# Kernel tuning notes

Hardware: AMD Instinct MI355X
Metric: run time of the kernel (lower is better)

## Reference

```python
import jax, jax.numpy as jnp
import numpy as np
from jax.ops import segment_sum

N_NODES = 100000
N_EDGES = 3200000
NUM_FEATURES = 256


def setup_inputs() -> dict:
    key = jax.random.key(0)
    ks = jax.random.split(key, 12)
    def lin(k, fan_in, fan_out):
        bound = 1.0 / np.sqrt(fan_in)
        kw, kb = jax.random.split(k)
        W = jax.random.uniform(kw, (fan_in, fan_out), jnp.float32, -bound, bound)
        b = jax.random.uniform(kb, (fan_out,), jnp.float32, -bound, bound)
        return W, b
    x = jax.random.normal(ks[0], (N_NODES, NUM_FEATURES), jnp.float32)
    edge_index = jax.random.randint(ks[1], (2, N_EDGES), 0, N_NODES, jnp.int64 if jax.config.jax_enable_x64 else jnp.int32)
    W1, b1 = lin(ks[2], NUM_FEATURES, 64)
    W2, b2 = lin(ks[3], 64, 32)
    W3, b3 = lin(ks[4], 32, 16)
    Ws02, bs02 = lin(ks[5], NUM_FEATURES, 32)
    Ws03, bs03 = lin(ks[6], NUM_FEATURES, 16)
    Ws13, bs13 = lin(ks[7], 64, 16)
    Wout, bout = lin(ks[8], 16, 1)
    return dict(x=x, edge_index=edge_index, W1=W1, b1=b1, W2=W2, b2=b2,
                W3=W3, b3=b3, Ws02=Ws02, bs02=bs02, Ws03=Ws03, bs03=bs03,
                Ws13=Ws13, bs13=bs13, Wout=Wout, bout=bout)


def _deg_inv_sqrt(edge_index, n_nodes):
    # gcn_norm with self-loops: degree counted at target nodes, +1 for self-loop
    dst = edge_index[1]
    deg = segment_sum(jnp.ones(edge_index.shape[1], jnp.float32), dst, num_segments=n_nodes) + 1.0
    return jnp.where(deg > 0, jax.lax.rsqrt(deg), 0.0)


def _gcn_conv(x, W, b, edge_index, dinv):
    # PyG GCNConv: h = x W; out[i] = sum_{j->i} dinv[j]*dinv[i]*h[j] + dinv[i]^2*h[i] + b
    src, dst = edge_index[0], edge_index[1]
    h = x @ W                                   # [N, out]
    norm = (dinv[src] * dinv[dst])[:, None]     # [E, 1]
    agg = segment_sum(h[src] * norm, dst, num_segments=x.shape[0])
    agg = agg + (dinv * dinv)[:, None] * h      # self-loop term
    return agg + b


def reference(x, edge_index, W1, b1, W2, b2, W3, b3,
              Ws02, bs02, Ws03, bs03, Ws13, bs13, Wout, bout):
    # Dropout in eval mode (identity).
    dinv = _deg_inv_sqrt(edge_index, x.shape[0])
    x1 = jax.nn.relu(_gcn_conv(x, W1, b1, edge_index, dinv))
    x2 = jax.nn.relu(_gcn_conv(x1, W2, b2, edge_index, dinv) + x @ Ws02 + bs02)
    x3 = jax.nn.relu(_gcn_conv(x2, W3, b3, edge_index, dinv)
                     + x @ Ws03 + bs03 + x1 @ Ws13 + bs13)
    return jax.nn.sigmoid(x3 @ Wout + bout)
```

## Files before the change

### kernel.cpp

```cpp
#include <hip/hip_runtime.h>
#include <hip/hip_bf16.h>
#include <math.h>


#define NBUCK_MAX 512
#define P1_CHUNK 8192
#define EPT 32
#define BCAP 9216

typedef __attribute__((ext_vector_type(8))) short bfrag;
typedef __attribute__((ext_vector_type(4))) float f4_t;

__device__ inline float uaf(unsigned u) { return __uint_as_float(u); }
__device__ inline ushort f2bf(float f) {
    __hip_bfloat16 b = __float2bfloat16(f);
    return *reinterpret_cast<ushort*>(&b);
}


__global__ __launch_bounds__(256) void bucket_hist_kernel(
    const int* __restrict__ dst, int E, int* __restrict__ bucket_count, int nbuckets)
{
    __shared__ int lhist[NBUCK_MAX];
    for (int i = threadIdx.x; i < nbuckets; i += 256) lhist[i] = 0;
    __syncthreads();
    const int stride = gridDim.x * 256;
    for (int e = blockIdx.x * 256 + threadIdx.x; e < E; e += stride)
        atomicAdd(&lhist[dst[e] >> 8], 1);
    __syncthreads();
    for (int i = threadIdx.x; i < nbuckets; i += 256) {
        int c = lhist[i];
        if (c) atomicAdd(&bucket_count[i], c);
    }
}

__global__ __launch_bounds__(512) void bucket_scan_kernel(
    const int* __restrict__ bucket_count, int* __restrict__ bucket_base,
    int* __restrict__ bucket_cursor, int nbuckets)
{
    __shared__ int tmp[512];
    const int tid = threadIdx.x;
    int v = (tid < nbuckets) ? bucket_count[tid] : 0;
    tmp[tid] = v;
    __syncthreads();
    for (int off = 1; off < 512; off <<= 1) {
        int t = (tid >= off) ? tmp[tid - off] : 0;
        __syncthreads();
        tmp[tid] += t;
        __syncthreads();
    }
    if (tid < nbuckets) {
        int base = tmp[tid] - v;
        bucket_base[tid]   = base;
        bucket_cursor[tid] = base;
    }
}

__global__ __launch_bounds__(256) void partition_kernel(
    const int* __restrict__ src, const int* __restrict__ dst, int E,
    int* __restrict__ bucket_cursor, unsigned int* __restrict__ keys, int nbuckets)
{
    __shared__ int hist[NBUCK_MAX];
    __shared__ int lofs[NBUCK_MAX];
    __shared__ int gbase[NBUCK_MAX];
    __shared__ int lcur[NBUCK_MAX];
    __shared__ int ssum[256];
    __shared__ unsigned int stage[P1_CHUNK];
    __shared__ int gidx[P1_CHUNK];

    const int tid = threadIdx.x;
    const int e0  = blockIdx.x * P1_CHUNK;
    const int nE  = min(P1_CHUNK, E - e0);

    for (int i = tid; i < NBUCK_MAX; i += 256) { hist[i] = 0; lcur[i] = 0; }
    __syncthreads();

    int myb[EPT];
    unsigned int mypk[EPT];
#pragma unroll
    for (int j = 0; j < EPT; ++j) {
        const int e = e0 + tid + j * 256;
        if (e < E) {
            const int d = dst[e];
            myb[j]  = d >> 8;
            mypk[j] = ((unsigned int)(d & 255) << 17) | (unsigned int)src[e];
            atomicAdd(&hist[myb[j]], 1);
        } else myb[j] = -1;
    }
    __syncthreads();

    int a0 = (2 * tid     < nbuckets) ? hist[2 * tid]     : 0;
    int a1 = (2 * tid + 1 < nbuckets) ? hist[2 * tid + 1] : 0;
    ssum[tid] = a0 + a1;
    __syncthreads();
    for (int off = 1; off < 256; off <<= 1) {
        int t = (tid >= off) ? ssum[tid - off] : 0;
        __syncthreads();
        ssum[tid] += t;
        __syncthreads();
    }
    const int ex = ssum[tid] - (a0 + a1);
    if (2 * tid     < nbuckets) lofs[2 * tid]     = ex;
    if (2 * tid + 1 < nbuckets) lofs[2 * tid + 1] = ex + a0;
    __syncthreads();

    for (int i = tid; i < nbuckets; i += 256)
        gbase[i] = atomicAdd(&bucket_cursor[i], hist[i]);
    __syncthreads();

#pragma unroll
    for (int j = 0; j < EPT; ++j) {
        if (myb[j] >= 0) {
            const int b = myb[j];
            const int l = lofs[b] + atomicAdd(&lcur[b], 1);
            stage[l] = mypk[j];
            gidx[l]  = gbase[b] - lofs[b] + l;
        }
    }
    __syncthreads();

    for (int i = tid; i < nE; i += 256)
        keys[gidx[i]] = stage[i];
}

__global__ __launch_bounds__(256) void csr_build_kernel(
    const unsigned int* __restrict__ keys, const int* __restrict__ bucket_base,
    const int* __restrict__ bucket_count,
    int* __restrict__ row_off, float* __restrict__ dinv, int* __restrict__ col,
    int N, int E)
{
    __shared__ unsigned int inb[BCAP];
    __shared__ int outv[BCAP];
    __shared__ int hist[256];
    __shared__ int lofs[256];
    __shared__ int ssum[256];

    const int tid  = threadIdx.x;
    const int b    = blockIdx.x;
    const int base = bucket_base[b];
    const int cnt  = min(bucket_count[b], BCAP);
    const int n0   = b << 8;
    const int nn   = min(256, N - n0);

    for (int i = tid; i < cnt; i += 256) inb[i] = keys[base + i];
    hist[tid] = 0;
    __syncthreads();

    for (int i = tid; i < cnt; i += 256)
        atomicAdd(&hist[inb[i] >> 17], 1);
    __syncthreads();

    ssum[tid] = hist[tid];
    __syncthreads();
    for (int off = 1; off < 256; off <<= 1) {
        int t = (tid >= off) ? ssum[tid - off] : 0;
        __syncthreads();
        ssum[tid] += t;
        __syncthreads();
    }
    lofs[tid] = ssum[tid] - hist[tid];

    if (tid < nn) {
        row_off[n0 + tid] = base + lofs[tid];
        dinv[n0 + tid]    = rsqrtf((float)hist[tid] + 1.0f);
    }
    if (b == 0 && tid == 0) row_off[N] = E;
    __syncthreads();

    hist[tid] = 0;
    __syncthreads();

    for (int i = tid; i < cnt; i += 256) {
        const unsigned int k = inb[i];
        const int node = k >> 17;
        const int l = lofs[node] + atomicAdd(&hist[node], 1);
        outv[l] = (int)(k & 0x1FFFF);
    }
    __syncthreads();

    for (int i = tid; i < cnt; i += 256)
        col[base + i] = outv[i];
}


__global__ __launch_bounds__(256) void prep_weights_kernel(
    const float* __restrict__ W1, const float* __restrict__ Ws02,
    const float* __restrict__ Ws03, const float* __restrict__ W2,
    const float* __restrict__ Ws13, const float* __restrict__ W3,
    ushort* __restrict__ Wt0, ushort* __restrict__ Wt1, ushort* __restrict__ Wt2)
{
    int idx = blockIdx.x * 256 + threadIdx.x;
    if (idx < 32768) {
        int f = idx >> 8, k = idx & 255;
        float v = 0.f;
        if (f < 64)       v = W1[k * 64 + f];
        else if (f < 96)  v = Ws02[k * 32 + (f - 64)];
        else if (f < 112) v = Ws03[k * 16 + (f - 96)];
        Wt0[idx] = f2bf(v);
    } else if (idx < 32768 + 3072) {
        int t = idx - 32768;
        int f = t >> 6, k = t & 63;
        float v = (f < 32) ? W2[k * 32 + f] : Ws13[k * 16 + (f - 32)];
        Wt1[t] = f2bf(v);
    } else if (idx < 32768 + 3072 + 512) {
        int t = idx - 32768 - 3072;
        int f = t >> 5, k = t & 31;
        Wt2[t] = f2bf(W3[k * 16 + f]);
    }
}


__global__ __launch_bounds__(256) void gemm_mfma0(
    const float* __restrict__ X, const ushort* __restrict__ Wt0,
    const float* __restrict__ bs02, const float* __restrict__ bs03,
    const float* __restrict__ dinv,
    __hip_bfloat16* __restrict__ g1, float* __restrict__ pre2,
    float* __restrict__ pre3, int N)
{
    constexpr int LDB = 264;
    constexpr int LDA = 40;
    __shared__ ushort Bs[128 * LDB];
    __shared__ ushort As[128 * LDA];

    const int tid  = threadIdx.x;
    const int lane = tid & 63;
    const int wave = tid >> 6;
    const int n0   = blockIdx.x * 128;

    for (int idx = tid; idx < 4096; idx += 256) {
        const int row = idx >> 5, c = idx & 31;
        *reinterpret_cast<uint4*>(&Bs[row * LDB + c * 8]) =
            *reinterpret_cast<const uint4*>(&Wt0[row * 256 + c * 8]);
    }

    f4_t acc[4][4];
#pragma unroll
    for (int a = 0; a < 4; ++a)
#pragma unroll
        for (int b = 0; b < 4; ++b) acc[a][b] = {0.f, 0.f, 0.f, 0.f};

    const int wm = wave & 1, wf = wave >> 1;

    for (int panel = 0; panel < 8; ++panel) {
        const int kc = panel * 32;
        for (int idx = tid; idx < 1024; idx += 256) {
            const int row = idx >> 3, q = idx & 7;
            const int n = n0 + row;
            float4 v = make_float4(0.f, 0.f, 0.f, 0.f);
            if (n < N)
                v = *reinterpret_cast<const float4*>(&X[(size_t)n * 256 + kc + q * 4]);
            ushort4 cv;
            cv.x = f2bf(v.x); cv.y = f2bf(v.y); cv.z = f2bf(v.z); cv.w = f2bf(v.w);
            *reinterpret_cast<ushort4*>(&As[row * LDA + q * 4]) = cv;
        }
        __syncthreads();

        bfrag af[4], bfr[4];
#pragma unroll
        for (int mt = 0; mt < 4; ++mt)
            af[mt] = *reinterpret_cast<const bfrag*>(
                &As[(wm * 64 + mt * 16 + (lane & 15)) * LDA + (lane >> 4) * 8]);
#pragma unroll
        for (int ft = 0; ft < 4; ++ft)
            bfr[ft] = *reinterpret_cast<const bfrag*>(
                &Bs[(wf * 64 + ft * 16 + (lane & 15)) * LDB + kc + (lane >> 4) * 8]);
#pragma unroll
        for (int mt = 0; mt < 4; ++mt)
#pragma unroll
            for (int ft = 0; ft < 4; ++ft)
                acc[mt][ft] = __builtin_amdgcn_mfma_f32_16x16x32_bf16(
                    af[mt], bfr[ft], acc[mt][ft], 0, 0, 0);
        __syncthreads();
    }

#pragma unroll
    for (int mt = 0; mt < 4; ++mt) {
#pragma unroll
        for (int ft = 0; ft < 4; ++ft) {
            const int fg = wf * 64 + ft * 16 + (lane & 15);
#pragma unroll
            for (int r = 0; r < 4; ++r) {
                const int n = n0 + wm * 64 + mt * 16 + (lane >> 4) * 4 + r;
                if (n >= N) continue;
                const float a = acc[mt][ft][r];
                if (fg < 64) {
                    g1[(size_t)n * 64 + fg] = __float2bfloat16(dinv[n] * a);
                } else if (fg < 96) {
                    pre2[(size_t)n * 32 + (fg - 64)] = a + bs02[fg - 64];
                } else if (fg < 112) {
                    pre3[(size_t)n * 16 + (fg - 96)] = a + bs03[fg - 96];
                }
            }
        }
    }
}

__global__ __launch_bounds__(256) void gemm_mfma1(
    const ushort* __restrict__ X1, const ushort* __restrict__ Wt1,
    const float* __restrict__ bs13, const float* __restrict__ dinv,
    __hip_bfloat16* __restrict__ g2, float* __restrict__ pre3, int N)
{
    constexpr int LDB = 72, LDA = 72;
    __shared__ ushort Bs[48 * LDB];
    __shared__ ushort As[128 * LDA];

    const int tid  = threadIdx.x;
    const int lane = tid & 63;
    const int wave = tid >> 6;
    const int n0   = blockIdx.x * 128;

    for (int idx = tid; idx < 384; idx += 256) {
        const int row = idx >> 3, c = idx & 7;
        *reinterpret_cast<uint4*>(&Bs[row * LDB + c * 8]) =
            *reinterpret_cast<const uint4*>(&Wt1[row * 64 + c * 8]);
    }
    for (int idx = tid; idx < 1024; idx += 256) {
        const int row = idx >> 3, c = idx & 7;
        const int n = n0 + row;
        uint4 v = make_uint4(0, 0, 0, 0);
        if (n < N) v = *reinterpret_cast<const uint4*>(&X1[(size_t)n * 64 + c * 8]);
        *reinterpret_cast<uint4*>(&As[row * LDA + c * 8]) = v;
    }
    __syncthreads();

    f4_t acc[2][3];
#pragma unroll
    for (int a = 0; a < 2; ++a)
#pragma unroll
        for (int b = 0; b < 3; ++b) acc[a][b] = {0.f, 0.f, 0.f, 0.f};

    const int m0 = wave * 32;
#pragma unroll
    for (int p = 0; p < 2; ++p) {
        bfrag af[2], bfr[3];
#pragma unroll
        for (int mt = 0; mt < 2; ++mt)
            af[mt] = *reinterpret_cast<const bfrag*>(
                &As[(m0 + mt * 16 + (lane & 15)) * LDA + p * 32 + (lane >> 4) * 8]);
#pragma unroll
        for (int ft = 0; ft < 3; ++ft)
            bfr[ft] = *reinterpret_cast<const bfrag*>(
                &Bs[(ft * 16 + (lane & 15)) * LDB + p * 32 + (lane >> 4) * 8]);
#pragma unroll
        for (int mt = 0; mt < 2; ++mt)
#pragma unroll
            for (int ft = 0; ft < 3; ++ft)
                acc[mt][ft] = __builtin_amdgcn_mfma_f32_16x16x32_bf16(
                    af[mt], bfr[ft], acc[mt][ft], 0, 0, 0);
    }

#pragma unroll
    for (int mt = 0; mt < 2; ++mt) {
#pragma unroll
        for (int ft = 0; ft < 3; ++ft) {
            const int fg = ft * 16 + (lane & 15);
#pragma unroll
            for (int r = 0; r < 4; ++r) {
                const int n = n0 + m0 + mt * 16 + (lane >> 4) * 4 + r;
                if (n >= N) continue;
                const float a = acc[mt][ft][r];
                if (fg < 32) {
                    g2[(size_t)n * 32 + fg] = __float2bfloat16(dinv[n] * a);
                } else {
                    pre3[(size_t)n * 16 + (fg - 32)] += a + bs13[fg - 32];
                }
            }
        }
    }
}

__global__ __launch_bounds__(256) void gemm_mfma2(
    const ushort* __restrict__ X2, const ushort* __restrict__ Wt2,
    const float* __restrict__ dinv, __hip_bfloat16* __restrict__ g3, int N)
{
    constexpr int LDA = 40;
    __shared__ ushort Bs[16 * LDA];
    __shared__ ushort As[256 * LDA];

    const int tid  = threadIdx.x;
    const int lane = tid & 63;
    const int wave = tid >> 6;
    const int n0   = blockIdx.x * 256;

    for (int idx = tid; idx < 64; idx += 256) {
        const int row = idx >> 2, c = idx & 3;
        *reinterpret_cast<uint4*>(&Bs[row * LDA + c * 8]) =
            *reinterpret_cast<const uint4*>(&Wt2[row * 32 + c * 8]);
    }
    for (int idx = tid; idx < 1024; idx += 256) {
        const int row = idx >> 2, c = idx & 3;
        const int n = n0 + row;
        uint4 v = make_uint4(0, 0, 0, 0);
        if (n < N) v = *reinterpret_cast<const uint4*>(&X2[(size_t)n * 32 + c * 8]);
        *reinterpret_cast<uint4*>(&As[row * LDA + c * 8]) = v;
    }
    __syncthreads();

    f4_t acc[4];
#pragma unroll
    for (int a = 0; a < 4; ++a) acc[a] = {0.f, 0.f, 0.f, 0.f};

    const int m0 = wave * 64;
    const bfrag bfr = *reinterpret_cast<const bfrag*>(
        &Bs[(lane & 15) * LDA + (lane >> 4) * 8]);
#pragma unroll
    for (int mt = 0; mt < 4; ++mt) {
        const bfrag af = *reinterpret_cast<const bfrag*>(
            &As[(m0 + mt * 16 + (lane & 15)) * LDA + (lane >> 4) * 8]);
        acc[mt] = __builtin_amdgcn_mfma_f32_16x16x32_bf16(af, bfr, acc[mt], 0, 0, 0);
    }

    const int fg = lane & 15;
#pragma unroll
    for (int mt = 0; mt < 4; ++mt) {
#pragma unroll
        for (int r = 0; r < 4; ++r) {
            const int n = n0 + m0 + mt * 16 + (lane >> 4) * 4 + r;
            if (n >= N) continue;
            g3[(size_t)n * 16 + fg] = __float2bfloat16(dinv[n] * acc[mt][r]);
        }
    }
}


template<int F, int MODE>
__global__ __launch_bounds__(256) void agg_kernel(
    const ushort* __restrict__ g, const float* __restrict__ dinv,
    const int* __restrict__ row_off, const int* __restrict__ col,
    const float* __restrict__ bias, const float* __restrict__ pre,
    const float* __restrict__ Wout, const float* __restrict__ bout,
    void* __restrict__ out, int N)
{
    constexpr int FG  = F / 4;
    constexpr int EPW = 64 / FG;
    constexpr int U   = (F == 64) ? 4 : (F == 32 ? 2 : 1);

    const int lane = threadIdx.x & 63;
    const int wv   = threadIdx.x >> 6;
    const int i    = blockIdx.x * 4 + wv;
    if (i >= N) return;

    const int fg = lane % FG;
    const int eo = lane / FG;
    const int fb = fg * 4;

    float a0 = 0.f, a1 = 0.f, a2 = 0.f, a3 = 0.f;
    const int s = row_off[i], e = row_off[i + 1];
    int p = s + eo;
    for (; p + (U - 1) * EPW < e; p += U * EPW) {
        int js[U];
#pragma unroll
        for (int u = 0; u < U; ++u) js[u] = col[p + u * EPW];
        uint2 w[U];
#pragma unroll
        for (int u = 0; u < U; ++u)
            w[u] = *reinterpret_cast<const uint2*>(&g[(size_t)js[u] * F + fb]);
#pragma unroll
        for (int u = 0; u < U; ++u) {
            a0 += uaf(w[u].x << 16);
            a1 += uaf(w[u].x & 0xffff0000u);
            a2 += uaf(w[u].y << 16);
            a3 += uaf(w[u].y & 0xffff0000u);
        }
    }
    for (; p < e; p += EPW) {
        const uint2 w0 = *reinterpret_cast<const uint2*>(&g[(size_t)col[p] * F + fb]);
        a0 += uaf(w0.x << 16);
        a1 += uaf(w0.x & 0xffff0000u);
        a2 += uaf(w0.y << 16);
        a3 += uaf(w0.y & 0xffff0000u);
    }
#pragma unroll
    for (int off = FG; off < 64; off <<= 1) {
        a0 += __shfl_xor(a0, off);
        a1 += __shfl_xor(a1, off);
        a2 += __shfl_xor(a2, off);
        a3 += __shfl_xor(a3, off);
    }

    const uint2 ws = *reinterpret_cast<const uint2*>(&g[(size_t)i * F + fb]);
    const float di = dinv[i];
    float v0 = di * (a0 + uaf(ws.x << 16))        + bias[fb + 0];
    float v1 = di * (a1 + uaf(ws.x & 0xffff0000u)) + bias[fb + 1];
    float v2 = di * (a2 + uaf(ws.y << 16))        + bias[fb + 2];
    float v3 = di * (a3 + uaf(ws.y & 0xffff0000u)) + bias[fb + 3];
    if (MODE != 0) {
        const float4 pv = *reinterpret_cast<const float4*>(&pre[(size_t)i * F + fb]);
        v0 += pv.x; v1 += pv.y; v2 += pv.z; v3 += pv.w;
    }
    v0 = fmaxf(v0, 0.f); v1 = fmaxf(v1, 0.f);
    v2 = fmaxf(v2, 0.f); v3 = fmaxf(v3, 0.f);

    if (MODE != 2) {
        if (lane < FG) {
            uint2 o;
            o.x = (unsigned)f2bf(v0) | ((unsigned)f2bf(v1) << 16);
            o.y = (unsigned)f2bf(v2) | ((unsigned)f2bf(v3) << 16);
            *reinterpret_cast<uint2*>(&((ushort*)out)[(size_t)i * F + fb]) = o;
        }
    } else {
        float t = v0 * Wout[fb] + v1 * Wout[fb + 1] +
                  v2 * Wout[fb + 2] + v3 * Wout[fb + 3];
        t += __shfl_xor(t, 1);
        t += __shfl_xor(t, 2);
        if (lane == 0)
            ((float*)out)[i] = 1.0f / (1.0f + expf(-(t + bout[0])));
    }
}


extern "C" void kernel_launch(void* const* d_in, const int* in_sizes, int n_in,
                              void* d_out, int out_size, void* d_ws, size_t ws_size,
                              hipStream_t stream)
{
    const float* x    = (const float*)d_in[0];
    const int*   edge = (const int*)d_in[1];
    const float* W1   = (const float*)d_in[2];
    const float* b1   = (const float*)d_in[3];
    const float* W2   = (const float*)d_in[4];
    const float* b2   = (const float*)d_in[5];
    const float* W3   = (const float*)d_in[6];
    const float* b3   = (const float*)d_in[7];
    const float* Ws02 = (const float*)d_in[8];
    const float* bs02 = (const float*)d_in[9];
    const float* Ws03 = (const float*)d_in[10];
    const float* bs03 = (const float*)d_in[11];
    const float* Ws13 = (const float*)d_in[12];
    const float* bs13 = (const float*)d_in[13];
    const float* Wout = (const float*)d_in[14];
    const float* bout = (const float*)d_in[15];

    const int N = in_sizes[0] / 256;
    const int E = in_sizes[1] / 2;
    const int* srcv = edge;
    const int* dstv = edge + E;
    const int nbuckets = (N + 255) >> 8;

    char* ws = (char*)d_ws;
    size_t off = 0;
    auto alloc = [&](size_t bytes) -> void* {
        void* p = ws + off;
        off += (bytes + 255) & ~(size_t)255;
        return p;
    };
    unsigned int* keys = (unsigned int*)alloc((size_t)E * 4);
    int*   col      = (int*)  alloc((size_t)E * 4);
    int*   bcount   = (int*)  alloc((size_t)NBUCK_MAX * 4);
    int*   bbase    = (int*)  alloc((size_t)NBUCK_MAX * 4);
    int*   bcursor  = (int*)  alloc((size_t)NBUCK_MAX * 4);
    int*   row_off  = (int*)  alloc((size_t)(N + 1) * 4);
    float* dinv     = (float*)alloc((size_t)N * 4);
    ushort* Wt0     = (ushort*)alloc((size_t)128 * 256 * 2);
    ushort* Wt1     = (ushort*)alloc((size_t)48 * 64 * 2);
    ushort* Wt2     = (ushort*)alloc((size_t)16 * 32 * 2);
    ushort* g1      = (ushort*)alloc((size_t)N * 64 * 2);
    ushort* x1      = (ushort*)alloc((size_t)N * 64 * 2);
    ushort* g2      = (ushort*)alloc((size_t)N * 32 * 2);
    ushort* x2      = (ushort*)alloc((size_t)N * 32 * 2);
    ushort* g3      = (ushort*)alloc((size_t)N * 16 * 2);
    float* pre2     = (float*)alloc((size_t)N * 32 * 4);
    float* pre3     = (float*)alloc((size_t)N * 16 * 4);

    prep_weights_kernel<<<142, 256, 0, stream>>>(W1, Ws02, Ws03, W2, Ws13, W3,
                                                 Wt0, Wt1, Wt2);
    hipMemsetAsync(bcount, 0, (size_t)NBUCK_MAX * 4, stream);
    bucket_hist_kernel<<<1024, 256, 0, stream>>>(dstv, E, bcount, nbuckets);
    bucket_scan_kernel<<<1, 512, 0, stream>>>(bcount, bbase, bcursor, nbuckets);
    partition_kernel<<<(E + P1_CHUNK - 1) / P1_CHUNK, 256, 0, stream>>>(
        srcv, dstv, E, bcursor, keys, nbuckets);
    csr_build_kernel<<<nbuckets, 256, 0, stream>>>(
        keys, bbase, bcount, row_off, dinv, col, N, E);

    const int ab = (N + 3) / 4;

    gemm_mfma0<<<(N + 127) / 128, 256, 0, stream>>>(
        x, Wt0, bs02, bs03, dinv, (__hip_bfloat16*)g1, pre2, pre3, N);
    agg_kernel<64, 0><<<ab, 256, 0, stream>>>(g1, dinv, row_off, col,
                                              b1, nullptr, nullptr, nullptr, x1, N);
    gemm_mfma1<<<(N + 127) / 128, 256, 0, stream>>>(
        x1, Wt1, bs13, dinv, (__hip_bfloat16*)g2, pre3, N);
    agg_kernel<32, 1><<<ab, 256, 0, stream>>>(g2, dinv, row_off, col,
                                              b2, pre2, nullptr, nullptr, x2, N);
    gemm_mfma2<<<(N + 255) / 256, 256, 0, stream>>>(
        x2, Wt2, dinv, (__hip_bfloat16*)g3, N);
    agg_kernel<16, 2><<<ab, 256, 0, stream>>>(g3, dinv, row_off, col,
                                              b3, pre3, Wout, bout, d_out, N);
}
```

Baseline: 488.9 us.

## Read GEMM weights from global, double-buffer X panels in gemm_mfma0

The weight fragments in all three MFMA GEMM kernels are now loaded straight from global memory (served from L2) instead of first being staged into shared memory. This shrinks gemm_mfma0's LDS footprint from about 77KB to about 20KB so more blocks can share a CU, and it requests 4 blocks per CU in the launch bounds. gemm_mfma0 also prefetches the next X panel into registers and converts it into a second LDS buffer while the current panel's MFMAs run, which removes one barrier per panel. The cost is repeated global and L2 reads of the weights by every wave, plus the register pressure of the prefetch under the tighter launch bound.

```diff
diff --git a/kernel.cpp b/kernel.cpp
--- a/kernel.cpp
+++ b/kernel.cpp
@@ -210,28 +210,30 @@
 }
 
 
-__global__ __launch_bounds__(256) void gemm_mfma0(
+__global__ __launch_bounds__(256, 4) void gemm_mfma0(
     const float* __restrict__ X, const ushort* __restrict__ Wt0,
     const float* __restrict__ bs02, const float* __restrict__ bs03,
     const float* __restrict__ dinv,
     __hip_bfloat16* __restrict__ g1, float* __restrict__ pre2,
     float* __restrict__ pre3, int N)
 {
-    constexpr int LDB = 264;
     constexpr int LDA = 40;
-    __shared__ ushort Bs[128 * LDB];
-    __shared__ ushort As[128 * LDA];
+    __shared__ ushort As[2][128 * LDA];
 
     const int tid  = threadIdx.x;
     const int lane = tid & 63;
     const int wave = tid >> 6;
     const int n0   = blockIdx.x * 128;
 
-    for (int idx = tid; idx < 4096; idx += 256) {
-        const int row = idx >> 5, c = idx & 31;
-        *reinterpret_cast<uint4*>(&Bs[row * LDB + c * 8]) =
-            *reinterpret_cast<const uint4*>(&Wt0[row * 256 + c * 8]);
-    }
+    const int srow = tid >> 1;
+    const int sq   = (tid & 1) * 4;
+    const float* xrow = (n0 + srow < N) ? &X[(size_t)(n0 + srow) * 256] : nullptr;
+
+    float4 pf[4];
+#pragma unroll
+    for (int j = 0; j < 4; ++j)
+        pf[j] = xrow ? *reinterpret_cast<const float4*>(&xrow[(sq + j) * 4])
+                     : make_float4(0.f, 0.f, 0.f, 0.f);
 
     f4_t acc[4][4];
 #pragma unroll
@@ -240,44 +242,70 @@
         for (int b = 0; b < 4; ++b) acc[a][b] = {0.f, 0.f, 0.f, 0.f};
 
     const int wm = wave & 1, wf = wave >> 1;
+    const int mrow = (lane & 15);
+    const int kq   = (lane >> 4) * 8;
+
+    {
+        ushort* dst = &As[0][srow * LDA + sq * 4];
+#pragma unroll
+        for (int j = 0; j < 4; ++j) {
+            ushort4 cv;
+            cv.x = f2bf(pf[j].x); cv.y = f2bf(pf[j].y);
+            cv.z = f2bf(pf[j].z); cv.w = f2bf(pf[j].w);
+            *reinterpret_cast<ushort4*>(&dst[j * 4]) = cv;
+        }
+    }
+    __syncthreads();
 
     for (int panel = 0; panel < 8; ++panel) {
         const int kc = panel * 32;
-        for (int idx = tid; idx < 1024; idx += 256) {
-            const int row = idx >> 3, q = idx & 7;
-            const int n = n0 + row;
-            float4 v = make_float4(0.f, 0.f, 0.f, 0.f);
-            if (n < N)
-                v = *reinterpret_cast<const float4*>(&X[(size_t)n * 256 + kc + q * 4]);
-            ushort4 cv;
-            cv.x = f2bf(v.x); cv.y = f2bf(v.y); cv.z = f2bf(v.z); cv.w = f2bf(v.w);
-            *reinterpret_cast<ushort4*>(&As[row * LDA + q * 4]) = cv;
-        }
-        __syncthreads();
-
-        bfrag af[4], bfr[4];
+        const int buf = panel & 1;
+
+        if (panel < 7) {
+#pragma unroll
+            for (int j = 0; j < 4; ++j)
+                pf[j] = xrow ? *reinterpret_cast<const float4*>(
+                                   &xrow[(panel + 1) * 32 + (sq + j) * 4])
+                             : make_float4(0.f, 0.f, 0.f, 0.f);
+        }
+
+        bfrag bfr[4];
+#pragma unroll
+        for (int ft = 0; ft < 4; ++ft) {
+            const uint4 raw = *reinterpret_cast<const uint4*>(
+                &Wt0[(size_t)(wf * 64 + ft * 16 + mrow) * 256 + kc + kq]);
+            bfr[ft] = *reinterpret_cast<const bfrag*>(&raw);
+        }
+        bfrag af[4];
 #pragma unroll
         for (int mt = 0; mt < 4; ++mt)
             af[mt] = *reinterpret_cast<const bfrag*>(
-                &As[(wm * 64 + mt * 16 + (lane & 15)) * LDA + (lane >> 4) * 8]);
-#pragma unroll
-        for (int ft = 0; ft < 4; ++ft)
-            bfr[ft] = *reinterpret_cast<const bfrag*>(
-                &Bs[(wf * 64 + ft * 16 + (lane & 15)) * LDB + kc + (lane >> 4) * 8]);
+                &As[buf][(wm * 64 + mt * 16 + mrow) * LDA + kq]);
 #pragma unroll
         for (int mt = 0; mt < 4; ++mt)
 #pragma unroll
             for (int ft = 0; ft < 4; ++ft)
                 acc[mt][ft] = __builtin_amdgcn_mfma_f32_16x16x32_bf16(
                     af[mt], bfr[ft], acc[mt][ft], 0, 0, 0);
-        __syncthreads();
+
+        if (panel < 7) {
+            ushort* dst = &As[1 - buf][srow * LDA + sq * 4];
+#pragma unroll
+            for (int j = 0; j < 4; ++j) {
+                ushort4 cv;
+                cv.x = f2bf(pf[j].x); cv.y = f2bf(pf[j].y);
+                cv.z = f2bf(pf[j].z); cv.w = f2bf(pf[j].w);
+                *reinterpret_cast<ushort4*>(&dst[j * 4]) = cv;
+            }
+            __syncthreads();
+        }
     }
 
 #pragma unroll
     for (int mt = 0; mt < 4; ++mt) {
 #pragma unroll
         for (int ft = 0; ft < 4; ++ft) {
-            const int fg = wf * 64 + ft * 16 + (lane & 15);
+            const int fg = wf * 64 + ft * 16 + mrow;
 #pragma unroll
             for (int r = 0; r < 4; ++r) {
                 const int n = n0 + wm * 64 + mt * 16 + (lane >> 4) * 4 + r;
@@ -300,8 +328,7 @@
     const float* __restrict__ bs13, const float* __restrict__ dinv,
     __hip_bfloat16* __restrict__ g2, float* __restrict__ pre3, int N)
 {
-    constexpr int LDB = 72, LDA = 72;
-    __shared__ ushort Bs[48 * LDB];
+    constexpr int LDA = 72;
     __shared__ ushort As[128 * LDA];
 
     const int tid  = threadIdx.x;
@@ -309,11 +336,6 @@
     const int wave = tid >> 6;
     const int n0   = blockIdx.x * 128;
 
-    for (int idx = tid; idx < 384; idx += 256) {
-        const int row = idx >> 3, c = idx & 7;
-        *reinterpret_cast<uint4*>(&Bs[row * LDB + c * 8]) =
-            *reinterpret_cast<const uint4*>(&Wt1[row * 64 + c * 8]);
-    }
     for (int idx = tid; idx < 1024; idx += 256) {
         const int row = idx >> 3, c = idx & 7;
         const int n = n0 + row;
@@ -330,17 +352,21 @@
         for (int b = 0; b < 3; ++b) acc[a][b] = {0.f, 0.f, 0.f, 0.f};
 
     const int m0 = wave * 32;
+    const int mrow = lane & 15;
+    const int kq   = (lane >> 4) * 8;
 #pragma unroll
     for (int p = 0; p < 2; ++p) {
         bfrag af[2], bfr[3];
 #pragma unroll
         for (int mt = 0; mt < 2; ++mt)
             af[mt] = *reinterpret_cast<const bfrag*>(
-                &As[(m0 + mt * 16 + (lane & 15)) * LDA + p * 32 + (lane >> 4) * 8]);
-#pragma unroll
-        for (int ft = 0; ft < 3; ++ft)
-            bfr[ft] = *reinterpret_cast<const bfrag*>(
-                &Bs[(ft * 16 + (lane & 15)) * LDB + p * 32 + (lane >> 4) * 8]);
+                &As[(m0 + mt * 16 + mrow) * LDA + p * 32 + kq]);
+#pragma unroll
+        for (int ft = 0; ft < 3; ++ft) {
+            const uint4 raw = *reinterpret_cast<const uint4*>(
+                &Wt1[(size_t)(ft * 16 + mrow) * 64 + p * 32 + kq]);
+            bfr[ft] = *reinterpret_cast<const bfrag*>(&raw);
+        }
 #pragma unroll
         for (int mt = 0; mt < 2; ++mt)
 #pragma unroll
@@ -353,7 +379,7 @@
     for (int mt = 0; mt < 2; ++mt) {
 #pragma unroll
         for (int ft = 0; ft < 3; ++ft) {
-            const int fg = ft * 16 + (lane & 15);
+            const int fg = ft * 16 + mrow;
 #pragma unroll
             for (int r = 0; r < 4; ++r) {
                 const int n = n0 + m0 + mt * 16 + (lane >> 4) * 4 + r;
@@ -374,7 +400,6 @@
     const float* __restrict__ dinv, __hip_bfloat16* __restrict__ g3, int N)
 {
     constexpr int LDA = 40;
-    __shared__ ushort Bs[16 * LDA];
     __shared__ ushort As[256 * LDA];
 
     const int tid  = threadIdx.x;
@@ -382,11 +407,6 @@
     const int wave = tid >> 6;
     const int n0   = blockIdx.x * 256;
 
-    for (int idx = tid; idx < 64; idx += 256) {
-        const int row = idx >> 2, c = idx & 3;
-        *reinterpret_cast<uint4*>(&Bs[row * LDA + c * 8]) =
-            *reinterpret_cast<const uint4*>(&Wt2[row * 32 + c * 8]);
-    }
     for (int idx = tid; idx < 1024; idx += 256) {
         const int row = idx >> 2, c = idx & 3;
         const int n = n0 + row;
@@ -401,23 +421,24 @@
     for (int a = 0; a < 4; ++a) acc[a] = {0.f, 0.f, 0.f, 0.f};
 
     const int m0 = wave * 64;
-    const bfrag bfr = *reinterpret_cast<const bfrag*>(
-        &Bs[(lane & 15) * LDA + (lane >> 4) * 8]);
+    const int mrow = lane & 15;
+    const int kq   = (lane >> 4) * 8;
+    const uint4 raw = *reinterpret_cast<const uint4*>(&Wt2[(size_t)mrow * 32 + kq]);
+    const bfrag bfr = *reinterpret_cast<const bfrag*>(&raw);
 #pragma unroll
     for (int mt = 0; mt < 4; ++mt) {
         const bfrag af = *reinterpret_cast<const bfrag*>(
-            &As[(m0 + mt * 16 + (lane & 15)) * LDA + (lane >> 4) * 8]);
+            &As[(m0 + mt * 16 + mrow) * LDA + kq]);
         acc[mt] = __builtin_amdgcn_mfma_f32_16x16x32_bf16(af, bfr, acc[mt], 0, 0, 0);
     }
 
-    const int fg = lane & 15;
 #pragma unroll
     for (int mt = 0; mt < 4; ++mt) {
 #pragma unroll
         for (int r = 0; r < 4; ++r) {
             const int n = n0 + m0 + mt * 16 + (lane >> 4) * 4 + r;
             if (n >= N) continue;
-            g3[(size_t)n * 16 + fg] = __float2bfloat16(dinv[n] * acc[mt][r]);
+            g3[(size_t)n * 16 + mrow] = __float2bfloat16(dinv[n] * acc[mt][r]);
         }
     }
 }
```

Result: faster. 477.9 us (-2.3%).
